# Optimization experiments

Hardware: AMD Instinct MI355X
Metric: run time of the kernel (lower is better)

Reference implementation:

```python
import jax, jax.numpy as jnp
import numpy as np

# pywt db2 decomposition filters
DEC_LO = np.array([-0.12940952255092145, 0.22414386804185735,
                   0.8365163037378079, 0.4829629131445341], dtype=np.float32)
DEC_HI = np.array([-0.4829629131445341, 0.8365163037378079,
                   -0.22414386804185735, -0.12940952255092145], dtype=np.float32)
LEVEL = 3
REC_WEIGHT = 1.0
FILT_LEN = 4
PAD = (2 * FILT_LEN - 3) // 2  # = 2, ptwt reflect padding per side


def _filters(dtype):
    # ptwt uses cross-correlation with flipped pywt filters (== true convolution)
    lo = jnp.asarray(DEC_LO[::-1].copy(), dtype=dtype)
    hi = jnp.asarray(DEC_HI[::-1].copy(), dtype=dtype)
    ll = jnp.outer(lo, lo)  # 'a'
    lh = jnp.outer(hi, lo)  # 'h'
    hl = jnp.outer(lo, hi)  # 'v'
    hh = jnp.outer(hi, hi)  # 'd'
    return jnp.stack([ll, lh, hl, hh])[:, None]  # [4,1,4,4]


def _dwt_step(x, filt):
    # x: [N, nb, H, W] -> [N, 4*nb, H', W'] (each band split into a,h,v,d; grouped)
    n, nb, h, w = x.shape
    padb = PAD + (h % 2)
    padr = PAD + (w % 2)
    xp = jnp.pad(x, ((0, 0), (0, 0), (PAD, padb), (PAD, padr)), mode='reflect')
    k = jnp.tile(filt, (nb, 1, 1, 1))  # [4*nb, 1, 4, 4]
    return jax.lax.conv_general_dilated(
        xp, k, window_strides=(2, 2), padding='VALID',
        feature_group_count=nb,
        dimension_numbers=('NCHW', 'OIHW', 'NCHW'))


def setup_inputs() -> dict:
    key = jax.random.key(0)
    k1, k2 = jax.random.split(key)
    preds = jax.random.normal(k1, (64, 3, 512, 512), dtype=jnp.float32)
    targets = jax.random.normal(k2, (64, 3, 512, 512), dtype=jnp.float32)
    return {"preds": preds, "targets": targets}


def reference(preds, targets):
    n, c, h, w = preds.shape
    p = preds.reshape(n * c, 1, h, w)
    t = targets.reshape(n * c, 1, h, w)
    filt = _filters(preds.dtype)
    for _ in range(LEVEL):
        p = _dwt_step(p, filt)
        t = _dwt_step(t, filt)
    # p, t: [N*C, 4**LEVEL, h', w']; leaf 0 is the all-'a' (pure approx) packet
    per_leaf_mse = jnp.mean((p - t) ** 2, axis=(0, 2, 3))  # [4**LEVEL]
    wvec = jnp.ones(per_leaf_mse.shape[0], dtype=preds.dtype).at[0].set(0.5)
    return REC_WEIGHT * jnp.dot(wvec, per_leaf_mse)
```

## Files before the change

kernel.cpp:

```cpp
#include <hip/hip_runtime.h>

#define F_LO0 0.4829629131445341f
#define F_LO1 0.8365163037378079f
#define F_LO2 0.22414386804185735f
#define F_LO3 (-0.12940952255092145f)
#define F_HI0 (-0.12940952255092145f)
#define F_HI1 (-0.22414386804185735f)
#define F_HI2 0.8365163037378079f
#define F_HI3 (-0.4829629131445341f)

__device__ __forceinline__ int reflect_idx(int r, int n) {
    r = (r < 0) ? -r : r;
    r = (r >= n) ? 2 * n - 2 - r : r;
    return r;
}

__device__ __forceinline__ void dwt4_pair(const float* __restrict__ s, int base,
                                          int stride, float o[2][4]) {
    float sl[2][4], sh[2][4];
#pragma unroll
    for (int u = 0; u < 4; ++u) {
        const float2 x0 = *(const float2*)(s + base + u * stride);
        const float2 x1 = *(const float2*)(s + base + u * stride + 2);
        const float2 x2 = *(const float2*)(s + base + u * stride + 4);
        sl[0][u] = F_LO0 * x0.x + F_LO1 * x0.y + F_LO2 * x1.x + F_LO3 * x1.y;
        sh[0][u] = F_HI0 * x0.x + F_HI1 * x0.y + F_HI2 * x1.x + F_HI3 * x1.y;
        sl[1][u] = F_LO0 * x1.x + F_LO1 * x1.y + F_LO2 * x2.x + F_LO3 * x2.y;
        sh[1][u] = F_HI0 * x1.x + F_HI1 * x1.y + F_HI2 * x2.x + F_HI3 * x2.y;
    }
#pragma unroll
    for (int q = 0; q < 2; ++q) {
        o[q][0] = F_LO0 * sl[q][0] + F_LO1 * sl[q][1] + F_LO2 * sl[q][2] + F_LO3 * sl[q][3];
        o[q][1] = F_HI0 * sl[q][0] + F_HI1 * sl[q][1] + F_HI2 * sl[q][2] + F_HI3 * sl[q][3];
        o[q][2] = F_LO0 * sh[q][0] + F_LO1 * sh[q][1] + F_LO2 * sh[q][2] + F_LO3 * sh[q][3];
        o[q][3] = F_HI0 * sh[q][0] + F_HI1 * sh[q][1] + F_HI2 * sh[q][2] + F_HI3 * sh[q][3];
    }
}

__global__ void __launch_bounds__(256) k_wpt_fused(
    const float* __restrict__ p, const float* __restrict__ t,
    float* __restrict__ out_sum, float inv_den) {
    constexpr int N0 = 512, N1 = 257, N2 = 130, N3 = 66;
    constexpr int S0 = 78;
    constexpr int S1 = 38, P1 = 38 * 38;
    constexpr int S2 = 20, P2 = 18 * 20;

    __shared__ float s_in[78 * 78];
    __shared__ float s_l1[4 * P1];
    float* const s_l2 = s_in;

    int bid = blockIdx.x;
    int swz = (bid & 7) * (int)(gridDim.x >> 3) + (bid >> 3);
    int img = swz / 81;
    int tt = swz - img * 81;
    int A = (tt / 9) * 8;
    int B = (tt % 9) * 8;

    const int tid = threadIdx.x;
    const size_t ibase = (size_t)img * (N0 * N0);

    const int O0r = 8 * A - 14, O0c = 8 * B - 14;
    const int O1r = 4 * A - 6, O1c = 4 * B - 6;
    const int O2r = 2 * A - 2, O2c = 2 * B - 2;

    const bool edge0 = (O0r < 0) || (O0r + 77 > 511) || (O0c < 0) || (O0c + 77 > 511);
    const bool edge1 = (O1r < 0) || (O1r + 37 > 256) || (O1c < 0) || (O1c + 37 > 256);
    const bool edge2 = (O2r < 0) || (O2r + 17 > 129) || (O2c < 0) || (O2c + 17 > 129);

    if (!edge0) {
        const float* prow = p + ibase + (size_t)O0r * N0 + O0c;
        const float* trow = t + ibase + (size_t)O0r * N0 + O0c;
#pragma unroll
        for (int it = 0; it < 12; ++it) {
            int e = it * 256 + tid;
            if (e < 3042) {
                unsigned lr = (unsigned)e / 39u;
                int lc = (int)((unsigned)e - lr * 39u) * 2;
                const float2 pv = *(const float2*)(prow + (size_t)lr * N0 + lc);
                const float2 tv = *(const float2*)(trow + (size_t)lr * N0 + lc);
                *(float2*)(s_in + lr * S0 + lc) = make_float2(pv.x - tv.x, pv.y - tv.y);
            }
        }
    } else {
#pragma unroll
        for (int it = 0; it < 12; ++it) {
            int e = it * 256 + tid;
            if (e < 3042) {
                unsigned lr = (unsigned)e / 39u;
                int lc = (int)((unsigned)e - lr * 39u) * 2;
                int rr = reflect_idx(O0r + (int)lr, N0);
                int c0 = reflect_idx(O0c + lc, N0);
                int c1 = reflect_idx(O0c + lc + 1, N0);
                const float* pr = p + ibase + (size_t)rr * N0;
                const float* tr = t + ibase + (size_t)rr * N0;
                *(float2*)(s_in + lr * S0 + lc) =
                    make_float2(pr[c0] - tr[c0], pr[c1] - tr[c1]);
            }
        }
    }
    __syncthreads();

#pragma unroll
    for (int it = 0; it < 3; ++it) {
        int e = it * 256 + tid;
        if (e < 722) {
            unsigned lr = (unsigned)e / 19u;
            int lc = (int)((unsigned)e - lr * 19u) * 2;
            float o[2][4];
            dwt4_pair(s_in, (int)(2u * lr) * S0 + 2 * lc, S0, o);
            int slot = (int)lr * S1 + lc;
#pragma unroll
            for (int b = 0; b < 4; ++b)
                *(float2*)(s_l1 + b * P1 + slot) = make_float2(o[0][b], o[1][b]);
        }
    }
    __syncthreads();
    if (edge1) {
        for (int it = 0; it < 6; ++it) {
            int e = it * 256 + tid;
            if (e < P1) {
                unsigned lr = (unsigned)e / 38u;
                unsigned lc = (unsigned)e - lr * 38u;
                int sr = reflect_idx(O1r + (int)lr, N1) - O1r;
                int sc = reflect_idx(O1c + (int)lc, N1) - O1c;
                if ((sr != (int)lr || sc != (int)lc) &&
                    (unsigned)sr < 38u && (unsigned)sc < 38u) {
                    int dst = (int)lr * S1 + (int)lc;
                    int src = sr * S1 + sc;
#pragma unroll
                    for (int b = 0; b < 4; ++b) s_l1[b * P1 + dst] = s_l1[b * P1 + src];
                }
            }
        }
        __syncthreads();
    }

#pragma unroll
    for (int it = 0; it < 3; ++it) {
        int e = it * 256 + tid;
        if (e < 648) {
            unsigned band = (unsigned)e / 162u;
            unsigned rem = (unsigned)e - band * 162u;
            unsigned lr = rem / 9u;
            int lc = (int)(rem - lr * 9u) * 2;
            float o[2][4];
            dwt4_pair(s_l1 + band * P1, (int)(2u * lr) * S1 + 2 * lc, S1, o);
            int slot = (int)lr * S2 + lc;
#pragma unroll
            for (int f = 0; f < 4; ++f)
                *(float2*)(s_l2 + (band * 4 + f) * P2 + slot) =
                    make_float2(o[0][f], o[1][f]);
        }
    }
    __syncthreads();
    if (edge2) {
        for (int it = 0; it < 2; ++it) {
            int e = it * 256 + tid;
            if (e < 324) {
                unsigned lr = (unsigned)e / 18u;
                unsigned lc = (unsigned)e - lr * 18u;
                int sr = reflect_idx(O2r + (int)lr, N2) - O2r;
                int sc = reflect_idx(O2c + (int)lc, N2) - O2c;
                if ((sr != (int)lr || sc != (int)lc) &&
                    (unsigned)sr < 18u && (unsigned)sc < 18u) {
                    int dst = (int)lr * S2 + (int)lc;
                    int src = sr * S2 + sc;
#pragma unroll
                    for (int pb = 0; pb < 16; ++pb)
                        s_l2[pb * P2 + dst] = s_l2[pb * P2 + src];
                }
            }
        }
        __syncthreads();
    }

    float local = 0.f;
#pragma unroll
    for (int it = 0; it < 2; ++it) {
        int e = it * 256 + tid;
        int b2 = e >> 5;
        int rem = e & 31;
        int pi = rem >> 2;
        int pj = (rem & 3) * 2;
        float o[2][4];
        dwt4_pair(s_l2 + b2 * P2, (2 * pi) * S2 + 2 * pj, S2, o);
        float w0 = (b2 == 0) ? 0.5f : 1.0f;
        bool rok = (A + pi < N3);
#pragma unroll
        for (int q = 0; q < 2; ++q) {
            if (rok && (B + pj + q < N3)) {
                local += w0 * o[q][0] * o[q][0] + o[q][1] * o[q][1] +
                         o[q][2] * o[q][2] + o[q][3] * o[q][3];
            }
        }
    }

#pragma unroll
    for (int off = 32; off > 0; off >>= 1) local += __shfl_down(local, off, 64);
    __shared__ float wsum[4];
    int wave = tid >> 6;
    if ((tid & 63) == 0) wsum[wave] = local;
    __syncthreads();
    if (tid == 0) {
        float s = (wsum[0] + wsum[1] + wsum[2] + wsum[3]) * inv_den;
        atomicAdd(out_sum, s);
    }
}

extern "C" void kernel_launch(void* const* d_in, const int* in_sizes, int n_in,
                              void* d_out, int out_size, void* d_ws, size_t ws_size,
                              hipStream_t stream) {
    const float* preds = (const float*)d_in[0];
    const float* targets = (const float*)d_in[1];
    float* out = (float*)d_out;

    hipMemsetAsync(d_out, 0, sizeof(float), stream);

    const float inv_den = 1.0f / (192.0f * 66.0f * 66.0f);
    const int nblk = 192 * 9 * 9;

    k_wpt_fused<<<dim3(nblk), dim3(256), 0, stream>>>(preds, targets, out, inv_den);
}
```

Baseline: 242.7 us.

## Split 2D DWT into separable row/column passes with even/odd deinterleaved shared layout

```diff
diff --git a/kernel.cpp b/kernel.cpp
--- a/kernel.cpp
+++ b/kernel.cpp
@@ -15,53 +15,28 @@
     return r;
 }
 
-__device__ __forceinline__ void dwt4_pair(const float* __restrict__ s, int base,
-                                          int stride, float o[2][4]) {
-    float sl[2][4], sh[2][4];
-#pragma unroll
-    for (int u = 0; u < 4; ++u) {
-        const float2 x0 = *(const float2*)(s + base + u * stride);
-        const float2 x1 = *(const float2*)(s + base + u * stride + 2);
-        const float2 x2 = *(const float2*)(s + base + u * stride + 4);
-        sl[0][u] = F_LO0 * x0.x + F_LO1 * x0.y + F_LO2 * x1.x + F_LO3 * x1.y;
-        sh[0][u] = F_HI0 * x0.x + F_HI1 * x0.y + F_HI2 * x1.x + F_HI3 * x1.y;
-        sl[1][u] = F_LO0 * x1.x + F_LO1 * x1.y + F_LO2 * x2.x + F_LO3 * x2.y;
-        sh[1][u] = F_HI0 * x1.x + F_HI1 * x1.y + F_HI2 * x2.x + F_HI3 * x2.y;
-    }
-#pragma unroll
-    for (int q = 0; q < 2; ++q) {
-        o[q][0] = F_LO0 * sl[q][0] + F_LO1 * sl[q][1] + F_LO2 * sl[q][2] + F_LO3 * sl[q][3];
-        o[q][1] = F_HI0 * sl[q][0] + F_HI1 * sl[q][1] + F_HI2 * sl[q][2] + F_HI3 * sl[q][3];
-        o[q][2] = F_LO0 * sh[q][0] + F_LO1 * sh[q][1] + F_LO2 * sh[q][2] + F_LO3 * sh[q][3];
-        o[q][3] = F_HI0 * sh[q][0] + F_HI1 * sh[q][1] + F_HI2 * sh[q][2] + F_HI3 * sh[q][3];
-    }
-}
-
 __global__ void __launch_bounds__(256) k_wpt_fused(
     const float* __restrict__ p, const float* __restrict__ t,
     float* __restrict__ out_sum, float inv_den) {
     constexpr int N0 = 512, N1 = 257, N2 = 130, N3 = 66;
-    constexpr int S0 = 78;
-    constexpr int S1 = 38, P1 = 38 * 38;
-    constexpr int S2 = 20, P2 = 18 * 20;
-
-    __shared__ float s_in[78 * 78];
-    __shared__ float s_l1[4 * P1];
-    float* const s_l2 = s_in;
+
+    __shared__ float sA[6084];
+    __shared__ float sB[6084];
+    __shared__ float wsum[4];
 
     int bid = blockIdx.x;
     int swz = (bid & 7) * (int)(gridDim.x >> 3) + (bid >> 3);
     int img = swz / 81;
     int tt = swz - img * 81;
-    int A = (tt / 9) * 8;
-    int B = (tt % 9) * 8;
+    int TA = (tt / 9) * 8;
+    int TB = (tt % 9) * 8;
 
     const int tid = threadIdx.x;
     const size_t ibase = (size_t)img * (N0 * N0);
 
-    const int O0r = 8 * A - 14, O0c = 8 * B - 14;
-    const int O1r = 4 * A - 6, O1c = 4 * B - 6;
-    const int O2r = 2 * A - 2, O2c = 2 * B - 2;
+    const int O0r = 8 * TA - 14, O0c = 8 * TB - 14;
+    const int O1r = 4 * TA - 6, O1c = 4 * TB - 6;
+    const int O2r = 2 * TA - 2, O2c = 2 * TB - 2;
 
     const bool edge0 = (O0r < 0) || (O0r + 77 > 511) || (O0c < 0) || (O0c + 77 > 511);
     const bool edge1 = (O1r < 0) || (O1r + 37 > 256) || (O1c < 0) || (O1c + 37 > 256);
@@ -74,11 +49,12 @@
         for (int it = 0; it < 12; ++it) {
             int e = it * 256 + tid;
             if (e < 3042) {
-                unsigned lr = (unsigned)e / 39u;
-                int lc = (int)((unsigned)e - lr * 39u) * 2;
-                const float2 pv = *(const float2*)(prow + (size_t)lr * N0 + lc);
-                const float2 tv = *(const float2*)(trow + (size_t)lr * N0 + lc);
-                *(float2*)(s_in + lr * S0 + lc) = make_float2(pv.x - tv.x, pv.y - tv.y);
+                unsigned r = (unsigned)e / 39u;
+                int k = e - (int)(39u * r);
+                const float2 pv = *(const float2*)(prow + (size_t)r * N0 + 2 * k);
+                const float2 tv = *(const float2*)(trow + (size_t)r * N0 + 2 * k);
+                sA[e] = pv.x - tv.x;
+                sA[e + 3042] = pv.y - tv.y;
             }
         }
     } else {
@@ -86,49 +62,70 @@
         for (int it = 0; it < 12; ++it) {
             int e = it * 256 + tid;
             if (e < 3042) {
-                unsigned lr = (unsigned)e / 39u;
-                int lc = (int)((unsigned)e - lr * 39u) * 2;
-                int rr = reflect_idx(O0r + (int)lr, N0);
-                int c0 = reflect_idx(O0c + lc, N0);
-                int c1 = reflect_idx(O0c + lc + 1, N0);
+                unsigned r = (unsigned)e / 39u;
+                int k = e - (int)(39u * r);
+                int rr = reflect_idx(O0r + (int)r, N0);
+                int c0 = reflect_idx(O0c + 2 * k, N0);
+                int c1 = reflect_idx(O0c + 2 * k + 1, N0);
                 const float* pr = p + ibase + (size_t)rr * N0;
                 const float* tr = t + ibase + (size_t)rr * N0;
-                *(float2*)(s_in + lr * S0 + lc) =
-                    make_float2(pr[c0] - tr[c0], pr[c1] - tr[c1]);
-            }
-        }
-    }
-    __syncthreads();
-
-#pragma unroll
-    for (int it = 0; it < 3; ++it) {
-        int e = it * 256 + tid;
-        if (e < 722) {
-            unsigned lr = (unsigned)e / 19u;
-            int lc = (int)((unsigned)e - lr * 19u) * 2;
-            float o[2][4];
-            dwt4_pair(s_in, (int)(2u * lr) * S0 + 2 * lc, S0, o);
-            int slot = (int)lr * S1 + lc;
-#pragma unroll
-            for (int b = 0; b < 4; ++b)
-                *(float2*)(s_l1 + b * P1 + slot) = make_float2(o[0][b], o[1][b]);
+                sA[e] = pr[c0] - tr[c0];
+                sA[e + 3042] = pr[c1] - tr[c1];
+            }
+        }
+    }
+    __syncthreads();
+
+#pragma unroll
+    for (int it = 0; it < 12; ++it) {
+        int e = it * 256 + tid;
+        if (e < 2964) {
+            unsigned r = (unsigned)e / 38u;
+            int a0 = e + (int)r;
+            float Ec = sA[a0], Ec1 = sA[a0 + 1];
+            float Oc = sA[a0 + 3042], Oc1 = sA[a0 + 3043];
+            sB[a0] = F_LO0 * Ec + F_LO1 * Oc + F_LO2 * Ec1 + F_LO3 * Oc1;
+            sB[a0 + 3042] = F_HI0 * Ec + F_HI1 * Oc + F_HI2 * Ec1 + F_HI3 * Oc1;
+        }
+    }
+    __syncthreads();
+
+#pragma unroll
+    for (int it = 0; it < 6; ++it) {
+        int e = it * 256 + tid;
+        if (e < 1444) {
+            unsigned r2 = (unsigned)e / 38u;
+            int c = e - (int)(38u * r2);
+            int base = e + (int)(40u * r2);
+            float l0 = sB[base], l1 = sB[base + 39], l2 = sB[base + 78], l3 = sB[base + 117];
+            float h0 = sB[base + 3042], h1 = sB[base + 3081], h2 = sB[base + 3120], h3 = sB[base + 3159];
+            float b0 = F_LO0 * l0 + F_LO1 * l1 + F_LO2 * l2 + F_LO3 * l3;
+            float b1 = F_HI0 * l0 + F_HI1 * l1 + F_HI2 * l2 + F_HI3 * l3;
+            float b2 = F_LO0 * h0 + F_LO1 * h1 + F_LO2 * h2 + F_LO3 * h3;
+            float b3 = F_HI0 * h0 + F_HI1 * h1 + F_HI2 * h2 + F_HI3 * h3;
+            int wa = (int)r2 * 19 + (c >> 1) + (c & 1) * 722;
+            sA[wa] = b0;
+            sA[wa + 1444] = b1;
+            sA[wa + 2888] = b2;
+            sA[wa + 4332] = b3;
         }
     }
     __syncthreads();
     if (edge1) {
         for (int it = 0; it < 6; ++it) {
             int e = it * 256 + tid;
-            if (e < P1) {
+            if (e < 1444) {
                 unsigned lr = (unsigned)e / 38u;
-                unsigned lc = (unsigned)e - lr * 38u;
+                int lc = e - (int)(38u * lr);
                 int sr = reflect_idx(O1r + (int)lr, N1) - O1r;
-                int sc = reflect_idx(O1c + (int)lc, N1) - O1c;
-                if ((sr != (int)lr || sc != (int)lc) &&
-                    (unsigned)sr < 38u && (unsigned)sc < 38u) {
-                    int dst = (int)lr * S1 + (int)lc;
-                    int src = sr * S1 + sc;
-#pragma unroll
-                    for (int b = 0; b < 4; ++b) s_l1[b * P1 + dst] = s_l1[b * P1 + src];
+                int sc = reflect_idx(O1c + lc, N1) - O1c;
+                if ((sr != (int)lr || sc != lc) && (unsigned)sr < 38u && (unsigned)sc < 38u) {
+                    int d = (int)lr * 19 + (lc >> 1) + (lc & 1) * 722;
+                    int s = sr * 19 + (sc >> 1) + (sc & 1) * 722;
+                    sA[d] = sA[s];
+                    sA[d + 1444] = sA[s + 1444];
+                    sA[d + 2888] = sA[s + 2888];
+                    sA[d + 4332] = sA[s + 4332];
                 }
             }
         }
@@ -136,20 +133,42 @@
     }
 
 #pragma unroll
-    for (int it = 0; it < 3; ++it) {
-        int e = it * 256 + tid;
-        if (e < 648) {
-            unsigned band = (unsigned)e / 162u;
-            unsigned rem = (unsigned)e - band * 162u;
-            unsigned lr = rem / 9u;
-            int lc = (int)(rem - lr * 9u) * 2;
-            float o[2][4];
-            dwt4_pair(s_l1 + band * P1, (int)(2u * lr) * S1 + 2 * lc, S1, o);
-            int slot = (int)lr * S2 + lc;
-#pragma unroll
-            for (int f = 0; f < 4; ++f)
-                *(float2*)(s_l2 + (band * 4 + f) * P2 + slot) =
-                    make_float2(o[0][f], o[1][f]);
+    for (int it = 0; it < 11; ++it) {
+        int e = it * 256 + tid;
+        if (e < 2736) {
+            unsigned b = (unsigned)e / 684u;
+            unsigned rem = (unsigned)e - 684u * b;
+            unsigned r = rem / 18u;
+            int c2 = (int)rem - (int)(18u * r);
+            int ra = (int)(b * 1444u + r * 19u) + c2;
+            float Ec = sA[ra], Ec1 = sA[ra + 1];
+            float Oc = sA[ra + 722], Oc1 = sA[ra + 723];
+            sB[ra] = F_LO0 * Ec + F_LO1 * Oc + F_LO2 * Ec1 + F_LO3 * Oc1;
+            sB[ra + 722] = F_HI0 * Ec + F_HI1 * Oc + F_HI2 * Ec1 + F_HI3 * Oc1;
+        }
+    }
+    __syncthreads();
+
+#pragma unroll
+    for (int it = 0; it < 6; ++it) {
+        int e = it * 256 + tid;
+        if (e < 1296) {
+            unsigned b = (unsigned)e / 324u;
+            unsigned rem = (unsigned)e - 324u * b;
+            unsigned r2 = rem / 18u;
+            int c = (int)rem - (int)(18u * r2);
+            int base = (int)(b * 1444u + 38u * r2) + c;
+            float l0 = sB[base], l1 = sB[base + 19], l2 = sB[base + 38], l3 = sB[base + 57];
+            float h0 = sB[base + 722], h1 = sB[base + 741], h2 = sB[base + 760], h3 = sB[base + 779];
+            float b0 = F_LO0 * l0 + F_LO1 * l1 + F_LO2 * l2 + F_LO3 * l3;
+            float b1 = F_HI0 * l0 + F_HI1 * l1 + F_HI2 * l2 + F_HI3 * l3;
+            float b2 = F_LO0 * h0 + F_LO1 * h1 + F_LO2 * h2 + F_LO3 * h3;
+            float b3 = F_HI0 * h0 + F_HI1 * h1 + F_HI2 * h2 + F_HI3 * h3;
+            int wa = (int)(b * 1296u + r2 * 9u) + (c >> 1) + (c & 1) * 162;
+            sA[wa] = b0;
+            sA[wa + 324] = b1;
+            sA[wa + 648] = b2;
+            sA[wa + 972] = b3;
         }
     }
     __syncthreads();
@@ -158,46 +177,60 @@
             int e = it * 256 + tid;
             if (e < 324) {
                 unsigned lr = (unsigned)e / 18u;
-                unsigned lc = (unsigned)e - lr * 18u;
+                int lc = e - (int)(18u * lr);
                 int sr = reflect_idx(O2r + (int)lr, N2) - O2r;
-                int sc = reflect_idx(O2c + (int)lc, N2) - O2c;
-                if ((sr != (int)lr || sc != (int)lc) &&
-                    (unsigned)sr < 18u && (unsigned)sc < 18u) {
-                    int dst = (int)lr * S2 + (int)lc;
-                    int src = sr * S2 + sc;
-#pragma unroll
-                    for (int pb = 0; pb < 16; ++pb)
-                        s_l2[pb * P2 + dst] = s_l2[pb * P2 + src];
+                int sc = reflect_idx(O2c + lc, N2) - O2c;
+                if ((sr != (int)lr || sc != lc) && (unsigned)sr < 18u && (unsigned)sc < 18u) {
+                    int d = (int)lr * 9 + (lc >> 1) + (lc & 1) * 162;
+                    int s = sr * 9 + (sc >> 1) + (sc & 1) * 162;
+#pragma unroll
+                    for (int pp = 0; pp < 16; ++pp) sA[d + 324 * pp] = sA[s + 324 * pp];
                 }
             }
         }
         __syncthreads();
     }
 
+#pragma unroll
+    for (int it = 0; it < 9; ++it) {
+        int e = it * 256 + tid;
+        if (e < 2304) {
+            unsigned pl = (unsigned)e / 144u;
+            unsigned rem = (unsigned)e - 144u * pl;
+            unsigned r = rem >> 3;
+            int c3 = (int)(rem & 7u);
+            int ra = (int)(pl * 324u + r * 9u) + c3;
+            float Ec = sA[ra], Ec1 = sA[ra + 1];
+            float Oc = sA[ra + 162], Oc1 = sA[ra + 163];
+            sB[ra] = F_LO0 * Ec + F_LO1 * Oc + F_LO2 * Ec1 + F_LO3 * Oc1;
+            sB[ra + 162] = F_HI0 * Ec + F_HI1 * Oc + F_HI2 * Ec1 + F_HI3 * Oc1;
+        }
+    }
+    __syncthreads();
+
     float local = 0.f;
 #pragma unroll
-    for (int it = 0; it < 2; ++it) {
-        int e = it * 256 + tid;
-        int b2 = e >> 5;
-        int rem = e & 31;
-        int pi = rem >> 2;
-        int pj = (rem & 3) * 2;
-        float o[2][4];
-        dwt4_pair(s_l2 + b2 * P2, (2 * pi) * S2 + 2 * pj, S2, o);
-        float w0 = (b2 == 0) ? 0.5f : 1.0f;
-        bool rok = (A + pi < N3);
-#pragma unroll
-        for (int q = 0; q < 2; ++q) {
-            if (rok && (B + pj + q < N3)) {
-                local += w0 * o[q][0] * o[q][0] + o[q][1] * o[q][1] +
-                         o[q][2] * o[q][2] + o[q][3] * o[q][3];
-            }
+    for (int it = 0; it < 4; ++it) {
+        int e = it * 256 + tid;
+        int pl = e >> 6;
+        int pos = e & 63;
+        int i = pos >> 3;
+        int j = pos & 7;
+        int base = pl * 324 + 18 * i + j;
+        float l0 = sB[base], l1 = sB[base + 9], l2 = sB[base + 18], l3 = sB[base + 27];
+        float h0 = sB[base + 162], h1 = sB[base + 171], h2 = sB[base + 180], h3 = sB[base + 189];
+        float o0 = F_LO0 * l0 + F_LO1 * l1 + F_LO2 * l2 + F_LO3 * l3;
+        float o1 = F_HI0 * l0 + F_HI1 * l1 + F_HI2 * l2 + F_HI3 * l3;
+        float o2 = F_LO0 * h0 + F_LO1 * h1 + F_LO2 * h2 + F_LO3 * h3;
+        float o3 = F_HI0 * h0 + F_HI1 * h1 + F_HI2 * h2 + F_HI3 * h3;
+        if (TA + i < N3 && TB + j < N3) {
+            float w0 = (pl == 0) ? 0.5f : 1.0f;
+            local += w0 * o0 * o0 + o1 * o1 + o2 * o2 + o3 * o3;
         }
     }
 
 #pragma unroll
     for (int off = 32; off > 0; off >>= 1) local += __shfl_down(local, off, 64);
-    __shared__ float wsum[4];
     int wave = tid >> 6;
     if ((tid & 63) == 0) wsum[wave] = local;
     __syncthreads();
```

After: 254.0 us. 1.05x slower.

## Split fused 2D DWT into separable row/column passes with float4 swizzled LDS

Applied to the files above, without the earlier changes.

```diff
diff --git a/kernel.cpp b/kernel.cpp
--- a/kernel.cpp
+++ b/kernel.cpp
@@ -15,120 +15,160 @@
     return r;
 }
 
-__device__ __forceinline__ void dwt4_pair(const float* __restrict__ s, int base,
-                                          int stride, float o[2][4]) {
-    float sl[2][4], sh[2][4];
-#pragma unroll
-    for (int u = 0; u < 4; ++u) {
-        const float2 x0 = *(const float2*)(s + base + u * stride);
-        const float2 x1 = *(const float2*)(s + base + u * stride + 2);
-        const float2 x2 = *(const float2*)(s + base + u * stride + 4);
-        sl[0][u] = F_LO0 * x0.x + F_LO1 * x0.y + F_LO2 * x1.x + F_LO3 * x1.y;
-        sh[0][u] = F_HI0 * x0.x + F_HI1 * x0.y + F_HI2 * x1.x + F_HI3 * x1.y;
-        sl[1][u] = F_LO0 * x1.x + F_LO1 * x1.y + F_LO2 * x2.x + F_LO3 * x2.y;
-        sh[1][u] = F_HI0 * x1.x + F_HI1 * x1.y + F_HI2 * x2.x + F_HI3 * x2.y;
-    }
-#pragma unroll
-    for (int q = 0; q < 2; ++q) {
-        o[q][0] = F_LO0 * sl[q][0] + F_LO1 * sl[q][1] + F_LO2 * sl[q][2] + F_LO3 * sl[q][3];
-        o[q][1] = F_HI0 * sl[q][0] + F_HI1 * sl[q][1] + F_HI2 * sl[q][2] + F_HI3 * sl[q][3];
-        o[q][2] = F_LO0 * sh[q][0] + F_LO1 * sh[q][1] + F_LO2 * sh[q][2] + F_LO3 * sh[q][3];
-        o[q][3] = F_HI0 * sh[q][0] + F_HI1 * sh[q][1] + F_HI2 * sh[q][2] + F_HI3 * sh[q][3];
-    }
+__device__ __forceinline__ float4 vfilt(const float4 a, const float4 b,
+                                        const float4 c, const float4 d,
+                                        float c0, float c1, float c2, float c3) {
+    return make_float4(c0 * a.x + c1 * b.x + c2 * c.x + c3 * d.x,
+                       c0 * a.y + c1 * b.y + c2 * c.y + c3 * d.y,
+                       c0 * a.z + c1 * b.z + c2 * c.z + c3 * d.z,
+                       c0 * a.w + c1 * b.w + c2 * c.w + c3 * d.w);
+}
+
+__device__ __forceinline__ void hfilt0(const float4 x0, const float4 x1, const float4 x2,
+                                       float4& lo, float4& hi) {
+    lo.x = F_LO0 * x0.x + F_LO1 * x0.y + F_LO2 * x0.z + F_LO3 * x0.w;
+    lo.y = F_LO0 * x0.z + F_LO1 * x0.w + F_LO2 * x1.x + F_LO3 * x1.y;
+    lo.z = F_LO0 * x1.x + F_LO1 * x1.y + F_LO2 * x1.z + F_LO3 * x1.w;
+    lo.w = F_LO0 * x1.z + F_LO1 * x1.w + F_LO2 * x2.x + F_LO3 * x2.y;
+    hi.x = F_HI0 * x0.x + F_HI1 * x0.y + F_HI2 * x0.z + F_HI3 * x0.w;
+    hi.y = F_HI0 * x0.z + F_HI1 * x0.w + F_HI2 * x1.x + F_HI3 * x1.y;
+    hi.z = F_HI0 * x1.x + F_HI1 * x1.y + F_HI2 * x1.z + F_HI3 * x1.w;
+    hi.w = F_HI0 * x1.z + F_HI1 * x1.w + F_HI2 * x2.x + F_HI3 * x2.y;
+}
+
+__device__ __forceinline__ void hfilt2(const float4 x0, const float4 x1, const float4 x2,
+                                       float4& lo, float4& hi) {
+    lo.x = F_LO0 * x0.z + F_LO1 * x0.w + F_LO2 * x1.x + F_LO3 * x1.y;
+    lo.y = F_LO0 * x1.x + F_LO1 * x1.y + F_LO2 * x1.z + F_LO3 * x1.w;
+    lo.z = F_LO0 * x1.z + F_LO1 * x1.w + F_LO2 * x2.x + F_LO3 * x2.y;
+    lo.w = F_LO0 * x2.x + F_LO1 * x2.y + F_LO2 * x2.z + F_LO3 * x2.w;
+    hi.x = F_HI0 * x0.z + F_HI1 * x0.w + F_HI2 * x1.x + F_HI3 * x1.y;
+    hi.y = F_HI0 * x1.x + F_HI1 * x1.y + F_HI2 * x1.z + F_HI3 * x1.w;
+    hi.z = F_HI0 * x1.z + F_HI1 * x1.w + F_HI2 * x2.x + F_HI3 * x2.y;
+    hi.w = F_HI0 * x2.x + F_HI1 * x2.y + F_HI2 * x2.z + F_HI3 * x2.w;
 }
 
 __global__ void __launch_bounds__(256) k_wpt_fused(
     const float* __restrict__ p, const float* __restrict__ t,
     float* __restrict__ out_sum, float inv_den) {
     constexpr int N0 = 512, N1 = 257, N2 = 130, N3 = 66;
-    constexpr int S0 = 78;
-    constexpr int S1 = 38, P1 = 38 * 38;
-    constexpr int S2 = 20, P2 = 18 * 20;
-
-    __shared__ float s_in[78 * 78];
-    __shared__ float s_l1[4 * P1];
-    float* const s_l2 = s_in;
+
+    __shared__ __align__(16) float sA[6240];
+    __shared__ __align__(16) float sB[6240];
+    __shared__ float wsum[4];
 
     int bid = blockIdx.x;
     int swz = (bid & 7) * (int)(gridDim.x >> 3) + (bid >> 3);
     int img = swz / 81;
     int tt = swz - img * 81;
-    int A = (tt / 9) * 8;
-    int B = (tt % 9) * 8;
+    int TA = (tt / 9) * 8;
+    int TB = (tt % 9) * 8;
 
     const int tid = threadIdx.x;
     const size_t ibase = (size_t)img * (N0 * N0);
 
-    const int O0r = 8 * A - 14, O0c = 8 * B - 14;
-    const int O1r = 4 * A - 6, O1c = 4 * B - 6;
-    const int O2r = 2 * A - 2, O2c = 2 * B - 2;
-
-    const bool edge0 = (O0r < 0) || (O0r + 77 > 511) || (O0c < 0) || (O0c + 77 > 511);
-    const bool edge1 = (O1r < 0) || (O1r + 37 > 256) || (O1c < 0) || (O1c + 37 > 256);
-    const bool edge2 = (O2r < 0) || (O2r + 17 > 129) || (O2c < 0) || (O2c + 17 > 129);
-
-    if (!edge0) {
-        const float* prow = p + ibase + (size_t)O0r * N0 + O0c;
-        const float* trow = t + ibase + (size_t)O0r * N0 + O0c;
-#pragma unroll
-        for (int it = 0; it < 12; ++it) {
+    const int O0r = 8 * TA - 14, O0c = 8 * TB - 16;
+    const int O1r = 4 * TA - 6, O1c = 4 * TB - 6;
+    const int O2r = 2 * TA - 2, O2c = 2 * TB - 2;
+    const bool edge = (TA == 0) || (TA == 64) || (TB == 0) || (TB == 64);
+
+    if (!edge) {
+        const float* __restrict__ pb = p + ibase + (size_t)O0r * N0 + O0c;
+        const float* __restrict__ tb = t + ibase + (size_t)O0r * N0 + O0c;
+#pragma unroll
+        for (int it = 0; it < 7; ++it) {
             int e = it * 256 + tid;
-            if (e < 3042) {
-                unsigned lr = (unsigned)e / 39u;
-                int lc = (int)((unsigned)e - lr * 39u) * 2;
-                const float2 pv = *(const float2*)(prow + (size_t)lr * N0 + lc);
-                const float2 tv = *(const float2*)(trow + (size_t)lr * N0 + lc);
-                *(float2*)(s_in + lr * S0 + lc) = make_float2(pv.x - tv.x, pv.y - tv.y);
+            if (e < 1560) {
+                int r = e / 20, q = e - r * 20;
+                const float4 pv = *(const float4*)(pb + (size_t)r * N0 + 4 * q);
+                const float4 tv = *(const float4*)(tb + (size_t)r * N0 + 4 * q);
+                *(float4*)(sA + r * 80 + ((q ^ (r & 1)) << 2)) =
+                    make_float4(pv.x - tv.x, pv.y - tv.y, pv.z - tv.z, pv.w - tv.w);
             }
         }
     } else {
 #pragma unroll
-        for (int it = 0; it < 12; ++it) {
+        for (int it = 0; it < 7; ++it) {
             int e = it * 256 + tid;
-            if (e < 3042) {
-                unsigned lr = (unsigned)e / 39u;
-                int lc = (int)((unsigned)e - lr * 39u) * 2;
-                int rr = reflect_idx(O0r + (int)lr, N0);
-                int c0 = reflect_idx(O0c + lc, N0);
-                int c1 = reflect_idx(O0c + lc + 1, N0);
-                const float* pr = p + ibase + (size_t)rr * N0;
-                const float* tr = t + ibase + (size_t)rr * N0;
-                *(float2*)(s_in + lr * S0 + lc) =
-                    make_float2(pr[c0] - tr[c0], pr[c1] - tr[c1]);
+            if (e < 1560) {
+                int r = e / 20, q = e - r * 20;
+                int gr = reflect_idx(O0r + r, N0);
+                const float* pr = p + ibase + (size_t)gr * N0;
+                const float* tr = t + ibase + (size_t)gr * N0;
+                float v[4];
+#pragma unroll
+                for (int x = 0; x < 4; ++x) {
+                    int gc = reflect_idx(O0c + 4 * q + x, N0);
+                    v[x] = pr[gc] - tr[gc];
+                }
+                *(float4*)(sA + r * 80 + ((q ^ (r & 1)) << 2)) =
+                    make_float4(v[0], v[1], v[2], v[3]);
             }
         }
     }
     __syncthreads();
 
 #pragma unroll
-    for (int it = 0; it < 3; ++it) {
-        int e = it * 256 + tid;
-        if (e < 722) {
-            unsigned lr = (unsigned)e / 19u;
-            int lc = (int)((unsigned)e - lr * 19u) * 2;
-            float o[2][4];
-            dwt4_pair(s_in, (int)(2u * lr) * S0 + 2 * lc, S0, o);
-            int slot = (int)lr * S1 + lc;
-#pragma unroll
-            for (int b = 0; b < 4; ++b)
-                *(float2*)(s_l1 + b * P1 + slot) = make_float2(o[0][b], o[1][b]);
-        }
-    }
-    __syncthreads();
-    if (edge1) {
+    for (int it = 0; it < 4; ++it) {
+        int e = it * 256 + tid;
+        if (e < 780) {
+            int r = e / 10, k = e - r * 10;
+            int r1 = r & 1;
+            const float* row = sA + r * 80;
+            int q2 = 2 * k + 2; if (q2 > 19) q2 = 18;
+            float4 x0 = *(const float4*)(row + (((2 * k) ^ r1) << 2));
+            float4 x1 = *(const float4*)(row + (((2 * k + 1) ^ r1) << 2));
+            float4 x2 = *(const float4*)(row + ((q2 ^ r1) << 2));
+            float4 lo, hi;
+            hfilt2(x0, x1, x2, lo, hi);
+            *(float4*)(sB + r * 40 + 4 * k) = lo;
+            *(float4*)(sB + 3120 + r * 40 + 4 * k) = hi;
+        }
+    }
+    __syncthreads();
+
+#pragma unroll
+    for (int it = 0; it < 2; ++it) {
+        int e = it * 256 + tid;
+        if (e < 380) {
+            int r1 = e / 10, k = e - r1 * 10;
+            const float* blo = sB + (2 * r1) * 40 + 4 * k;
+            const float* bhi = blo + 3120;
+            float4 L0 = *(const float4*)(blo);
+            float4 L1v = *(const float4*)(blo + 40);
+            float4 L2v = *(const float4*)(blo + 80);
+            float4 L3v = *(const float4*)(blo + 120);
+            float4 H0 = *(const float4*)(bhi);
+            float4 H1 = *(const float4*)(bhi + 40);
+            float4 H2 = *(const float4*)(bhi + 80);
+            float4 H3 = *(const float4*)(bhi + 120);
+            float4 b0 = vfilt(L0, L1v, L2v, L3v, F_LO0, F_LO1, F_LO2, F_LO3);
+            float4 b1 = vfilt(L0, L1v, L2v, L3v, F_HI0, F_HI1, F_HI2, F_HI3);
+            float4 b2 = vfilt(H0, H1, H2, H3, F_LO0, F_LO1, F_LO2, F_LO3);
+            float4 b3 = vfilt(H0, H1, H2, H3, F_HI0, F_HI1, F_HI2, F_HI3);
+            int wo = r1 * 40 + ((k ^ (r1 & 1)) << 2);
+            *(float4*)(sA + wo) = b0;
+            *(float4*)(sA + 1520 + wo) = b1;
+            *(float4*)(sA + 3040 + wo) = b2;
+            *(float4*)(sA + 4560 + wo) = b3;
+        }
+    }
+    __syncthreads();
+    if (edge) {
+#pragma unroll
         for (int it = 0; it < 6; ++it) {
             int e = it * 256 + tid;
-            if (e < P1) {
-                unsigned lr = (unsigned)e / 38u;
-                unsigned lc = (unsigned)e - lr * 38u;
-                int sr = reflect_idx(O1r + (int)lr, N1) - O1r;
-                int sc = reflect_idx(O1c + (int)lc, N1) - O1c;
-                if ((sr != (int)lr || sc != (int)lc) &&
-                    (unsigned)sr < 38u && (unsigned)sc < 38u) {
-                    int dst = (int)lr * S1 + (int)lc;
-                    int src = sr * S1 + sc;
-#pragma unroll
-                    for (int b = 0; b < 4; ++b) s_l1[b * P1 + dst] = s_l1[b * P1 + src];
+            if (e < 1444) {
+                int lr = e / 38, lc = e - lr * 38;
+                int sr = reflect_idx(O1r + lr, N1) - O1r;
+                int sc = reflect_idx(O1c + lc, N1) - O1c;
+                if ((sr != lr || sc != lc) && (unsigned)sr < 38u && (unsigned)sc < 38u) {
+                    int da = lr * 40 + ((((lc >> 2) ^ (lr & 1)) << 2) | (lc & 3));
+                    int sa = sr * 40 + ((((sc >> 2) ^ (sr & 1)) << 2) | (sc & 3));
+                    sA[da] = sA[sa];
+                    sA[1520 + da] = sA[1520 + sa];
+                    sA[3040 + da] = sA[3040 + sa];
+                    sA[4560 + da] = sA[4560 + sa];
                 }
             }
         }
@@ -138,66 +178,122 @@
 #pragma unroll
     for (int it = 0; it < 3; ++it) {
         int e = it * 256 + tid;
-        if (e < 648) {
-            unsigned band = (unsigned)e / 162u;
-            unsigned rem = (unsigned)e - band * 162u;
-            unsigned lr = rem / 9u;
-            int lc = (int)(rem - lr * 9u) * 2;
-            float o[2][4];
-            dwt4_pair(s_l1 + band * P1, (int)(2u * lr) * S1 + 2 * lc, S1, o);
-            int slot = (int)lr * S2 + lc;
-#pragma unroll
-            for (int f = 0; f < 4; ++f)
-                *(float2*)(s_l2 + (band * 4 + f) * P2 + slot) =
-                    make_float2(o[0][f], o[1][f]);
-        }
-    }
-    __syncthreads();
-    if (edge2) {
+        if (e < 760) {
+            int b = e / 190, rem = e - b * 190;
+            int r = rem / 5, k = rem - r * 5;
+            int r1 = r & 1;
+            const float* row = sA + b * 1520 + r * 40;
+            int q2 = 2 * k + 2; if (q2 > 9) q2 = 8;
+            float4 x0 = *(const float4*)(row + (((2 * k) ^ r1) << 2));
+            float4 x1 = *(const float4*)(row + (((2 * k + 1) ^ r1) << 2));
+            float4 x2 = *(const float4*)(row + ((q2 ^ r1) << 2));
+            float4 lo, hi;
+            hfilt0(x0, x1, x2, lo, hi);
+            float* dst = sB + b * 1520 + r * 20 + 4 * k;
+            *(float4*)dst = lo;
+            *(float4*)(dst + 760) = hi;
+        }
+    }
+    __syncthreads();
+
+#pragma unroll
+    for (int it = 0; it < 2; ++it) {
+        int e = it * 256 + tid;
+        if (e < 360) {
+            int b = e / 90, rem = e - b * 90;
+            int r2 = rem / 5, k = rem - r2 * 5;
+            const float* blo = sB + b * 1520 + (2 * r2) * 20 + 4 * k;
+            const float* bhi = blo + 760;
+            float4 L0 = *(const float4*)(blo);
+            float4 L1v = *(const float4*)(blo + 20);
+            float4 L2v = *(const float4*)(blo + 40);
+            float4 L3v = *(const float4*)(blo + 60);
+            float4 H0 = *(const float4*)(bhi);
+            float4 H1 = *(const float4*)(bhi + 20);
+            float4 H2 = *(const float4*)(bhi + 40);
+            float4 H3 = *(const float4*)(bhi + 60);
+            float4 b0 = vfilt(L0, L1v, L2v, L3v, F_LO0, F_LO1, F_LO2, F_LO3);
+            float4 b1 = vfilt(L0, L1v, L2v, L3v, F_HI0, F_HI1, F_HI2, F_HI3);
+            float4 b2 = vfilt(H0, H1, H2, H3, F_LO0, F_LO1, F_LO2, F_LO3);
+            float4 b3 = vfilt(H0, H1, H2, H3, F_HI0, F_HI1, F_HI2, F_HI3);
+            float* dst = sA + (b * 4) * 360 + r2 * 20 + 4 * k;
+            *(float4*)(dst) = b0;
+            *(float4*)(dst + 360) = b1;
+            *(float4*)(dst + 720) = b2;
+            *(float4*)(dst + 1080) = b3;
+        }
+    }
+    __syncthreads();
+    if (edge) {
+#pragma unroll
         for (int it = 0; it < 2; ++it) {
             int e = it * 256 + tid;
             if (e < 324) {
-                unsigned lr = (unsigned)e / 18u;
-                unsigned lc = (unsigned)e - lr * 18u;
-                int sr = reflect_idx(O2r + (int)lr, N2) - O2r;
-                int sc = reflect_idx(O2c + (int)lc, N2) - O2c;
-                if ((sr != (int)lr || sc != (int)lc) &&
-                    (unsigned)sr < 18u && (unsigned)sc < 18u) {
-                    int dst = (int)lr * S2 + (int)lc;
-                    int src = sr * S2 + sc;
-#pragma unroll
-                    for (int pb = 0; pb < 16; ++pb)
-                        s_l2[pb * P2 + dst] = s_l2[pb * P2 + src];
+                int lr = e / 18, lc = e - lr * 18;
+                int sr = reflect_idx(O2r + lr, N2) - O2r;
+                int sc = reflect_idx(O2c + lc, N2) - O2c;
+                if ((sr != lr || sc != lc) && (unsigned)sr < 18u && (unsigned)sc < 18u) {
+                    int d = lr * 20 + lc;
+                    int s = sr * 20 + sc;
+#pragma unroll
+                    for (int pp = 0; pp < 16; ++pp) sA[d + 360 * pp] = sA[s + 360 * pp];
                 }
             }
         }
         __syncthreads();
     }
 
+#pragma unroll
+    for (int it = 0; it < 3; ++it) {
+        int e = it * 256 + tid;
+        if (e < 576) {
+            int pl = e / 36, rem = e - pl * 36;
+            int r = rem >> 1, k = rem & 1;
+            const float* row = sA + pl * 360 + r * 20 + 8 * k;
+            float4 x0 = *(const float4*)(row);
+            float4 x1 = *(const float4*)(row + 4);
+            float4 x2 = *(const float4*)(row + 8);
+            float4 lo, hi;
+            hfilt0(x0, x1, x2, lo, hi);
+            float* dst = sB + pl * 296 + r * 8 + 4 * k;
+            *(float4*)dst = lo;
+            *(float4*)(dst + 148) = hi;
+        }
+    }
+    __syncthreads();
+
     float local = 0.f;
-#pragma unroll
-    for (int it = 0; it < 2; ++it) {
-        int e = it * 256 + tid;
-        int b2 = e >> 5;
-        int rem = e & 31;
-        int pi = rem >> 2;
-        int pj = (rem & 3) * 2;
-        float o[2][4];
-        dwt4_pair(s_l2 + b2 * P2, (2 * pi) * S2 + 2 * pj, S2, o);
-        float w0 = (b2 == 0) ? 0.5f : 1.0f;
-        bool rok = (A + pi < N3);
-#pragma unroll
-        for (int q = 0; q < 2; ++q) {
-            if (rok && (B + pj + q < N3)) {
-                local += w0 * o[q][0] * o[q][0] + o[q][1] * o[q][1] +
-                         o[q][2] * o[q][2] + o[q][3] * o[q][3];
-            }
+    {
+        int e = tid;
+        int pl = e >> 4;
+        int i = (e >> 1) & 7;
+        int k = e & 1;
+        const float* blo = sB + pl * 296 + (2 * i) * 8 + 4 * k;
+        const float* bhi = blo + 148;
+        float4 L0 = *(const float4*)(blo);
+        float4 L1v = *(const float4*)(blo + 8);
+        float4 L2v = *(const float4*)(blo + 16);
+        float4 L3v = *(const float4*)(blo + 24);
+        float4 H0 = *(const float4*)(bhi);
+        float4 H1 = *(const float4*)(bhi + 8);
+        float4 H2 = *(const float4*)(bhi + 16);
+        float4 H3 = *(const float4*)(bhi + 24);
+        float4 o0 = vfilt(L0, L1v, L2v, L3v, F_LO0, F_LO1, F_LO2, F_LO3);
+        float4 o1 = vfilt(L0, L1v, L2v, L3v, F_HI0, F_HI1, F_HI2, F_HI3);
+        float4 o2 = vfilt(H0, H1, H2, H3, F_LO0, F_LO1, F_LO2, F_LO3);
+        float4 o3 = vfilt(H0, H1, H2, H3, F_HI0, F_HI1, F_HI2, F_HI3);
+        float w0 = (pl == 0) ? 0.5f : 1.0f;
+        int jb = TB + 4 * k;
+        if (TA + i < N3) {
+            if (jb + 0 < N3) local += w0 * o0.x * o0.x + o1.x * o1.x + o2.x * o2.x + o3.x * o3.x;
+            if (jb + 1 < N3) local += w0 * o0.y * o0.y + o1.y * o1.y + o2.y * o2.y + o3.y * o3.y;
+            if (jb + 2 < N3) local += w0 * o0.z * o0.z + o1.z * o1.z + o2.z * o2.z + o3.z * o3.z;
+            if (jb + 3 < N3) local += w0 * o0.w * o0.w + o1.w * o1.w + o2.w * o2.w + o3.w * o3.w;
         }
     }
 
 #pragma unroll
     for (int off = 32; off > 0; off >>= 1) local += __shfl_down(local, off, 64);
-    __shared__ float wsum[4];
     int wave = tid >> 6;
     if ((tid & 63) == 0) wsum[wave] = local;
     __syncthreads();
```

Result: no change. 243.6 us (+0.4%).
